# Performance work log

Hardware: AMD Instinct MI355X
Metric: run time of the kernel (lower is better)

## Reference

```python
import jax, jax.numpy as jnp
import numpy as np

B = 8          # number of point clouds
P = 2048       # points per cloud (equal-length segments)
D_FEAT = 16    # matched feature dim
BIG = 1e10     # mask value for cross-batch pairs

LOSS_WEIGHT = 1.0
COORD_WEIGHT = 1.0
FEAT_WEIGHT = 0.1


def setup_inputs() -> dict:
    key = jax.random.key(0)
    k1, k2, k3, k4 = jax.random.split(key, 4)
    n = B * P
    pred_coord = jax.random.normal(k1, (n, 3), dtype=jnp.float32) * 10.0
    target_coord = jax.random.normal(k2, (n, 3), dtype=jnp.float32) * 10.0
    pred_feat = jax.random.normal(k3, (n, D_FEAT), dtype=jnp.float32)
    target_feat = jax.random.normal(k4, (n, D_FEAT), dtype=jnp.float32)
    offsets = (jnp.arange(1, B + 1) * P).astype(jnp.int32)  # cumulative ends
    return {
        'pred_coord': pred_coord,
        'target_coord': target_coord,
        'pred_feat': pred_feat,
        'target_feat': target_feat,
        'pred_offset': offsets,
        'target_offset': offsets,
    }


def _batch_ids(offsets, n):
    # point i belongs to batch b where offsets[b-1] <= i < offsets[b]
    return jnp.searchsorted(offsets, jnp.arange(n), side='right')


def _lengths(offsets):
    prev = jnp.concatenate([jnp.zeros((1,), offsets.dtype), offsets[:-1]])
    return offsets - prev


def _nn_dist(x, y, xb, yb):
    # masked all-pairs squared distances [n, m]; per-batch KNN(k=1)
    d2 = (jnp.sum(x * x, axis=1)[:, None]
          - 2.0 * (x @ y.T)
          + jnp.sum(y * y, axis=1)[None, :])
    d2 = jnp.where(xb[:, None] == yb[None, :], d2, BIG)
    idx = jnp.argmin(d2, axis=1)
    nearest = y[idx]                          # gather nearest neighbor
    dist = jnp.sum((x - nearest) ** 2, axis=1)  # norm=2, recomputed as in torch
    return dist, idx


def _chamfer_dir(x, y, x_off, y_off):
    xb = _batch_ids(x_off, x.shape[0])
    yb = _batch_ids(y_off, y.shape[0])
    dist, idx = _nn_dist(x, y, xb, yb)
    seg = jax.ops.segment_sum(dist, xb, num_segments=B)
    lens = jnp.maximum(_lengths(x_off), 1).astype(dist.dtype)
    return seg / lens, idx                    # point_reduction='mean'


def reference(pred_coord, target_coord, pred_feat, target_feat,
              pred_offset, target_offset):
    cham_x, x_idx = _chamfer_dir(pred_coord, target_coord, pred_offset, target_offset)
    cham_y, _ = _chamfer_dir(target_coord, pred_coord, target_offset, pred_offset)
    # bidirectional sum, batch_reduction='mean' (weights None -> divide by B)
    coord_loss = jnp.sum(cham_x + cham_y) / B
    # matched feature MSE via pred->target nearest-neighbor indices
    nearest_feat = target_feat[x_idx]
    feat_loss = jnp.mean((pred_feat - nearest_feat) ** 2)
    loss = LOSS_WEIGHT * (COORD_WEIGHT * coord_loss + FEAT_WEIGHT * feat_loss)
    return (loss, coord_loss, feat_loss)
```

## Files before the change

### kernel.cpp

```cpp
#include <hip/hip_runtime.h>

#define BATCHES 8
#define PTS     2048
#define DFEAT   16
#define NQ      16384
#define NBLK    512

__global__ __launch_bounds__(512, 4) void
nn_fused_kernel(const float* __restrict__ pred_coord,
                const float* __restrict__ target_coord,
                const float* __restrict__ pred_feat,
                const float* __restrict__ target_feat,
                float2* __restrict__ partials) {
    __shared__ float4 cand[2048];
    __shared__ unsigned long long pk[8][4][4][16];
    __shared__ unsigned long long fk[64];
    __shared__ float wa[8], wb[8];

    const int bid   = blockIdx.x;
    const int dir   = bid >> 8;
    const int rem   = bid & 255;
    const int batch = rem >> 5;
    const int qg    = rem & 31;
    const int tid   = threadIdx.x;
    const int lane  = tid & 63;
    const int slice = tid >> 6;
    const int g     = lane >> 4;
    const int q16   = lane & 15;

    const float* x = (dir == 0) ? pred_coord   : target_coord;
    const float* y = (dir == 0) ? target_coord : pred_coord;

    const float* ybase = y + (size_t)batch * PTS * 3;
    #pragma unroll
    for (int r = 0; r < 4; ++r) {
        int k = tid + 512 * r;
        float cx = ybase[3 * k], cy = ybase[3 * k + 1], cz = ybase[3 * k + 2];
        cand[k] = make_float4(cx, cy, cz, 0.5f * (cx * cx + cy * cy + cz * cz));
    }

    const int qbase = batch * PTS + qg * 64;
    float nax[4], nay[4], naz[4], hx[4];
    #pragma unroll
    for (int k = 0; k < 4; ++k) {
        int q = qbase + q16 + 16 * k;
        float ax = x[3 * q], ay = x[3 * q + 1], az = x[3 * q + 2];
        nax[k] = -ax; nay[k] = -ay; naz[k] = -az;
        hx[k]  = 0.5f * (ax * ax + ay * ay + az * az);
    }

    __syncthreads();

    const int jbase = slice * 256 + g;
    float best[4] = {1e30f, 1e30f, 1e30f, 1e30f};
    int   bj[4]   = {0, 0, 0, 0};
    if (dir == 0) {
        #pragma unroll 8
        for (int i = 0; i < 64; ++i) {
            int j = jbase + 4 * i;
            float4 c = cand[j];
            #pragma unroll
            for (int k = 0; k < 4; ++k) {
                float s = fmaf(nax[k], c.x,
                          fmaf(nay[k], c.y,
                          fmaf(naz[k], c.z, c.w)));
                if (s < best[k]) { best[k] = s; bj[k] = j; }
            }
        }
    } else {
        #pragma unroll 8
        for (int i = 0; i < 64; ++i) {
            float4 c = cand[jbase + 4 * i];
            #pragma unroll
            for (int k = 0; k < 4; ++k) {
                float s = fmaf(nax[k], c.x,
                          fmaf(nay[k], c.y,
                          fmaf(naz[k], c.z, c.w)));
                best[k] = fminf(best[k], s);
            }
        }
    }
    #pragma unroll
    for (int k = 0; k < 4; ++k) {
        pk[slice][g][k][q16] =
            ((unsigned long long)__float_as_uint(fmaxf(best[k] + hx[k], 0.f)) << 32)
            | (unsigned int)bj[k];
    }
    __syncthreads();

    float ds = 0.f, fs = 0.f;
    if (tid < 64) {
        unsigned long long m = ~0ull;
        #pragma unroll
        for (int w = 0; w < 8; ++w)
            #pragma unroll
            for (int gg = 0; gg < 4; ++gg) {
                unsigned long long v = pk[w][gg][tid >> 4][tid & 15];
                m = (v < m) ? v : m;
            }
        fk[tid] = m;
        ds = 2.0f * __uint_as_float((unsigned int)(m >> 32));
    }
    __syncthreads();

    if (dir == 0 && tid < 256) {
        const unsigned long long m = fk[tid >> 2];
        const int row = batch * PTS + (int)(m & 0xffffffffu);
        const float4* pf = (const float4*)(pred_feat + (size_t)(qbase + (tid >> 2)) * DFEAT);
        const float4* tf = (const float4*)(target_feat + (size_t)row * DFEAT);
        float4 a = pf[tid & 3], b = tf[tid & 3];
        float d0 = a.x - b.x, d1 = a.y - b.y, d2 = a.z - b.z, d3 = a.w - b.w;
        fs = d0 * d0 + d1 * d1 + d2 * d2 + d3 * d3;
    }

    #pragma unroll
    for (int off = 32; off > 0; off >>= 1) {
        ds += __shfl_down(ds, off);
        fs += __shfl_down(fs, off);
    }
    if (lane == 0) { wa[slice] = ds; wb[slice] = fs; }
    __syncthreads();
    if (tid == 0) {
        float a = 0.f, b = 0.f;
        #pragma unroll
        for (int w = 0; w < 8; ++w) { a += wa[w]; b += wb[w]; }
        partials[bid] = make_float2(a, b);
    }
}

__global__ __launch_bounds__(512) void
final_kernel(const float2* __restrict__ partials, float* __restrict__ out) {
    __shared__ float a8[8], b8[8];
    const int tid = threadIdx.x;
    float2 p = partials[tid];
    float ds = p.x, fs = p.y;
    #pragma unroll
    for (int off = 32; off > 0; off >>= 1) {
        ds += __shfl_down(ds, off);
        fs += __shfl_down(fs, off);
    }
    const int wave = tid >> 6, lane = tid & 63;
    if (lane == 0) { a8[wave] = ds; b8[wave] = fs; }
    __syncthreads();
    if (tid == 0) {
        float dsum = 0.f, fsum = 0.f;
        #pragma unroll
        for (int w = 0; w < 8; ++w) { dsum += a8[w]; fsum += b8[w]; }
        float coord_loss = dsum / (float)(BATCHES * PTS);
        float feat_loss  = fsum / (float)(NQ * DFEAT);
        out[0] = coord_loss + 0.1f * feat_loss;
        out[1] = coord_loss;
        out[2] = feat_loss;
    }
}

extern "C" void kernel_launch(void* const* d_in, const int* in_sizes, int n_in,
                              void* d_out, int out_size, void* d_ws, size_t ws_size,
                              hipStream_t stream) {
    const float* pred_coord   = (const float*)d_in[0];
    const float* target_coord = (const float*)d_in[1];
    const float* pred_feat    = (const float*)d_in[2];
    const float* target_feat  = (const float*)d_in[3];

    float2* partials = (float2*)d_ws;

    nn_fused_kernel<<<NBLK, 512, 0, stream>>>(pred_coord, target_coord,
                                              pred_feat, target_feat, partials);
    final_kernel<<<1, 512, 0, stream>>>(partials, (float*)d_out);
}
```

Baseline: 74.33 us.

## Halve queries per block, double grid, and reduce argmin keys with wave shuffles

Each block now handles 32 queries instead of 64, so the grid grows from 512 to 1024 blocks and launch bounds ask for 8 blocks per CU. Each wave is split into 8 candidate groups instead of 4. Per-thread argmin keys are combined across groups with xor shuffles before the shared-memory cross-wave reduction. Candidate coordinates are loaded with vectorized float4 reads. The aim is more parallelism and less LDS reduction traffic. The cost is that every block reloads the same 2048-candidate tile, so total staging work doubles, and the tighter register budget can cause spills.

```diff
diff --git a/kernel.cpp b/kernel.cpp
--- a/kernel.cpp
+++ b/kernel.cpp
@@ -4,46 +4,52 @@
 #define PTS     2048
 #define DFEAT   16
 #define NQ      16384
-#define NBLK    512
+#define NBLK    1024
 
-__global__ __launch_bounds__(512, 4) void
+__global__ __launch_bounds__(512, 8) void
 nn_fused_kernel(const float* __restrict__ pred_coord,
                 const float* __restrict__ target_coord,
                 const float* __restrict__ pred_feat,
                 const float* __restrict__ target_feat,
                 float2* __restrict__ partials) {
     __shared__ float4 cand[2048];
-    __shared__ unsigned long long pk[8][4][4][16];
-    __shared__ unsigned long long fk[64];
+    __shared__ unsigned long long pk[8][32];
+    __shared__ unsigned long long fk[32];
     __shared__ float wa[8], wb[8];
 
     const int bid   = blockIdx.x;
-    const int dir   = bid >> 8;
-    const int rem   = bid & 255;
-    const int batch = rem >> 5;
-    const int qg    = rem & 31;
+    const int dir   = bid >> 9;
+    const int rem   = bid & 511;
+    const int batch = rem >> 6;
+    const int qg    = rem & 63;
     const int tid   = threadIdx.x;
     const int lane  = tid & 63;
     const int slice = tid >> 6;
-    const int g     = lane >> 4;
-    const int q16   = lane & 15;
+    const int g     = lane >> 3;
+    const int q8    = lane & 7;
 
     const float* x = (dir == 0) ? pred_coord   : target_coord;
     const float* y = (dir == 0) ? target_coord : pred_coord;
 
-    const float* ybase = y + (size_t)batch * PTS * 3;
-    #pragma unroll
-    for (int r = 0; r < 4; ++r) {
-        int k = tid + 512 * r;
-        float cx = ybase[3 * k], cy = ybase[3 * k + 1], cz = ybase[3 * k + 2];
-        cand[k] = make_float4(cx, cy, cz, 0.5f * (cx * cx + cy * cy + cz * cz));
+    {
+        const float4* yv = (const float4*)(y + (size_t)batch * PTS * 3);
+        float4 p0 = yv[3 * tid], p1 = yv[3 * tid + 1], p2 = yv[3 * tid + 2];
+        float cx, cy, cz;
+        cx = p0.x; cy = p0.y; cz = p0.z;
+        cand[4 * tid + 0] = make_float4(cx, cy, cz, 0.5f * (cx*cx + cy*cy + cz*cz));
+        cx = p0.w; cy = p1.x; cz = p1.y;
+        cand[4 * tid + 1] = make_float4(cx, cy, cz, 0.5f * (cx*cx + cy*cy + cz*cz));
+        cx = p1.z; cy = p1.w; cz = p2.x;
+        cand[4 * tid + 2] = make_float4(cx, cy, cz, 0.5f * (cx*cx + cy*cy + cz*cz));
+        cx = p2.y; cy = p2.z; cz = p2.w;
+        cand[4 * tid + 3] = make_float4(cx, cy, cz, 0.5f * (cx*cx + cy*cy + cz*cz));
     }
 
-    const int qbase = batch * PTS + qg * 64;
+    const int qbase = batch * PTS + qg * 32;
     float nax[4], nay[4], naz[4], hx[4];
     #pragma unroll
     for (int k = 0; k < 4; ++k) {
-        int q = qbase + q16 + 16 * k;
+        int q = qbase + q8 + 8 * k;
         float ax = x[3 * q], ay = x[3 * q + 1], az = x[3 * q + 2];
         nax[k] = -ax; nay[k] = -ay; naz[k] = -az;
         hx[k]  = 0.5f * (ax * ax + ay * ay + az * az);
@@ -55,9 +61,9 @@
     float best[4] = {1e30f, 1e30f, 1e30f, 1e30f};
     int   bj[4]   = {0, 0, 0, 0};
     if (dir == 0) {
-        #pragma unroll 8
-        for (int i = 0; i < 64; ++i) {
-            int j = jbase + 4 * i;
+        #pragma unroll 4
+        for (int i = 0; i < 32; ++i) {
+            int j = jbase + 8 * i;
             float4 c = cand[j];
             #pragma unroll
             for (int k = 0; k < 4; ++k) {
@@ -68,9 +74,9 @@
             }
         }
     } else {
-        #pragma unroll 8
-        for (int i = 0; i < 64; ++i) {
-            float4 c = cand[jbase + 4 * i];
+        #pragma unroll 4
+        for (int i = 0; i < 32; ++i) {
+            float4 c = cand[jbase + 8 * i];
             #pragma unroll
             for (int k = 0; k < 4; ++k) {
                 float s = fmaf(nax[k], c.x,
@@ -80,30 +86,42 @@
             }
         }
     }
+
+    unsigned long long key[4];
     #pragma unroll
     for (int k = 0; k < 4; ++k) {
-        pk[slice][g][k][q16] =
-            ((unsigned long long)__float_as_uint(fmaxf(best[k] + hx[k], 0.f)) << 32)
-            | (unsigned int)bj[k];
+        key[k] = ((unsigned long long)
+                  __float_as_uint(fmaxf(best[k] + hx[k], 0.f)) << 32)
+                 | (unsigned int)bj[k];
+    }
+    #pragma unroll
+    for (int m = 8; m <= 32; m <<= 1) {
+        #pragma unroll
+        for (int k = 0; k < 4; ++k) {
+            unsigned long long v = __shfl_xor(key[k], m);
+            key[k] = (v < key[k]) ? v : key[k];
+        }
+    }
+    if (g == 0) {
+        #pragma unroll
+        for (int k = 0; k < 4; ++k) pk[slice][q8 + 8 * k] = key[k];
     }
     __syncthreads();
 
     float ds = 0.f, fs = 0.f;
-    if (tid < 64) {
-        unsigned long long m = ~0ull;
+    if (tid < 32) {
+        unsigned long long m = pk[0][tid];
         #pragma unroll
-        for (int w = 0; w < 8; ++w)
-            #pragma unroll
-            for (int gg = 0; gg < 4; ++gg) {
-                unsigned long long v = pk[w][gg][tid >> 4][tid & 15];
-                m = (v < m) ? v : m;
-            }
+        for (int c = 1; c < 8; ++c) {
+            unsigned long long v = pk[c][tid];
+            m = (v < m) ? v : m;
+        }
         fk[tid] = m;
         ds = 2.0f * __uint_as_float((unsigned int)(m >> 32));
     }
     __syncthreads();
 
-    if (dir == 0 && tid < 256) {
+    if (dir == 0 && tid < 128) {
         const unsigned long long m = fk[tid >> 2];
         const int row = batch * PTS + (int)(m & 0xffffffffu);
         const float4* pf = (const float4*)(pred_feat + (size_t)(qbase + (tid >> 2)) * DFEAT);
@@ -132,8 +150,9 @@
 final_kernel(const float2* __restrict__ partials, float* __restrict__ out) {
     __shared__ float a8[8], b8[8];
     const int tid = threadIdx.x;
-    float2 p = partials[tid];
-    float ds = p.x, fs = p.y;
+    float2 p0 = partials[tid];
+    float2 p1 = partials[tid + 512];
+    float ds = p0.x + p1.x, fs = p0.y + p1.y;
     #pragma unroll
     for (int off = 32; off > 0; off >>= 1) {
         ds += __shfl_down(ds, off);
```

New measurement: 73.97 us. About the same (-0.5%).
